# Performance work log

Hardware: AMD Instinct MI355X
Metric: run time of the kernel (lower is better)

Reference implementation:

```python
import jax, jax.numpy as jnp
import numpy as np

E = 1024  # embedding_dim
H = 64    # head_size

def setup_inputs() -> dict:
    key = jax.random.key(0)
    k1, k2, k3, k4 = jax.random.split(key, 4)
    x = jax.random.normal(k1, (4, 4096, E), dtype=jnp.float32)
    # nn.Linear(E, H, bias=False) weights have shape [H, E]; y = x @ W.T
    s = 1.0 / np.sqrt(E)
    Wq = jax.random.normal(k2, (H, E), dtype=jnp.float32) * s
    Wk = jax.random.normal(k3, (H, E), dtype=jnp.float32) * s
    Wv = jax.random.normal(k4, (H, E), dtype=jnp.float32) * s
    return {"x": x, "Wq": Wq, "Wk": Wk, "Wv": Wv}

def reference(x, Wq, Wk, Wv):
    B, T, E_ = x.shape
    q = jnp.einsum('bte,he->bth', x, Wq)
    k = jnp.einsum('bte,he->bth', x, Wk)
    v = jnp.einsum('bte,he->bth', x, Wv)
    # NOTE: original scales by sqrt(embedding_dim), not head_size
    scores = jnp.einsum('bqh,bkh->bqk', q, k) / jnp.sqrt(jnp.asarray(E_, x.dtype))
    causal = jnp.tril(jnp.ones((T, T), dtype=bool))
    scores = jnp.where(causal, scores, -jnp.inf)
    weights = jax.nn.softmax(scores, axis=-1)
    return jnp.einsum('bqk,bkh->bqh', weights, v)
```

## Files before the change

kernel.cpp:

```cpp
#include <hip/hip_runtime.h>
#include <stdint.h>

typedef __bf16 bf16x8 __attribute__((ext_vector_type(8)));
typedef float  f32x4  __attribute__((ext_vector_type(4)));

#define E_DIM 1024
#define H_DIM 64
#define T_SEQ 4096
#define B_BAT 4
#define M_TOT (B_BAT * T_SEQ)

__device__ __forceinline__ ushort f2bfu(float f) {
    return __builtin_bit_cast(ushort, (__bf16)f);
}
__device__ __forceinline__ uint32_t pk2(float lo, float hi) {
    return (uint32_t)f2bfu(lo) | ((uint32_t)f2bfu(hi) << 16);
}
__device__ __forceinline__ float ex2(float x) {
    return __builtin_amdgcn_exp2f(x);
}
__device__ __forceinline__ bf16x8 ldfrag(const ushort* p) {
    return __builtin_bit_cast(bf16x8, *(const uint4*)(p));
}
__device__ __forceinline__ void barrier_lgkm() {
    __builtin_amdgcn_s_waitcnt(0xC07F);
    __builtin_amdgcn_s_barrier();
}

__global__ __launch_bounds__(256) void wcvt(const float* __restrict__ Wq,
                                            const float* __restrict__ Wk,
                                            const float* __restrict__ Wv,
                                            ushort* __restrict__ Wfm) {
    int g = blockIdx.x * 256 + threadIdx.x;
    int n = g >> 7;
    int k8 = g & 127;
    const float* src = (n < 64) ? (Wq + (size_t)n * E_DIM)
                     : (n < 128) ? (Wk + (size_t)(n - 64) * E_DIM)
                     : (Wv + (size_t)(n - 128) * E_DIM);
    float sc = (n < 64) ? 0.045084220f : 1.0f;
    float4 a = *(const float4*)(src + k8 * 8);
    float4 b = *(const float4*)(src + k8 * 8 + 4);
    uint4 o;
    o.x = pk2(a.x * sc, a.y * sc); o.y = pk2(a.z * sc, a.w * sc);
    o.z = pk2(b.x * sc, b.y * sc); o.w = pk2(b.z * sc, b.w * sc);
    int s = k8 >> 3, kc = (k8 >> 2) & 1, qd = k8 & 3;
    int nt = n >> 4, lm = n & 15;
    int lane = qd * 16 + lm;
    *(uint4*)(Wfm + (((size_t)(s * 12 + nt) * 2 + kc) * 64 + lane) * 8) = o;
}

__global__ __launch_bounds__(256, 3) void qkv(const float* __restrict__ x,
                                              const ushort* __restrict__ Wfm,
                                              ushort* __restrict__ Qfm,
                                              ushort* __restrict__ Kfm,
                                              ushort* __restrict__ Vfm) {
    __shared__ union {
        ushort a[2][32 * 72];
        struct { ushort c[32 * 136]; ushort vt[64 * 40]; } epi;
    } sm;
    const int tid = threadIdx.x;
    const int w = tid >> 6, l = tid & 63;
    const int lm = l & 15, qd = l >> 4;
    const int m0 = blockIdx.x * 32;

    f32x4 acc[2][3];
#pragma unroll
    for (int r2 = 0; r2 < 2; ++r2)
#pragma unroll
        for (int t = 0; t < 3; ++t) acc[r2][t] = (f32x4){0.f, 0.f, 0.f, 0.f};

    const int srow = tid >> 3, kseg = tid & 7;
    const float* xsrc = x + (size_t)(m0 + srow) * E_DIM + kseg * 8;

    {
        float4 a0 = *(const float4*)xsrc;
        float4 a1 = *(const float4*)(xsrc + 4);
        uint4 u = {pk2(a0.x, a0.y), pk2(a0.z, a0.w), pk2(a1.x, a1.y), pk2(a1.z, a1.w)};
        *(uint4*)(&sm.a[0][srow * 72 + kseg * 8]) = u;
    }
    float4 xa0 = *(const float4*)(xsrc + 64);
    float4 xa1 = *(const float4*)(xsrc + 68);
    float4 xb0 = *(const float4*)(xsrc + 128);
    float4 xb1 = *(const float4*)(xsrc + 132);
    __syncthreads();

    for (int s = 0; s < 16; ++s) {
        const int cb = s & 1, nb = cb ^ 1;
        float4 xc0 = xa0, xc1 = xa1;
        if (s < 13) {
            xc0 = *(const float4*)(xsrc + (s + 3) * 64);
            xc1 = *(const float4*)(xsrc + (s + 3) * 64 + 4);
        }
        bf16x8 wf[3][2];
#pragma unroll
        for (int t = 0; t < 3; ++t)
#pragma unroll
            for (int kc = 0; kc < 2; ++kc)
                wf[t][kc] = ldfrag(Wfm + (((size_t)(s * 12 + w * 3 + t) * 2 + kc) * 64 + l) * 8);
        bf16x8 af[2][2];
#pragma unroll
        for (int r2 = 0; r2 < 2; ++r2)
#pragma unroll
            for (int kc = 0; kc < 2; ++kc)
                af[r2][kc] = ldfrag(&sm.a[cb][(r2 * 16 + lm) * 72 + kc * 32 + qd * 8]);
#pragma unroll
        for (int t = 0; t < 3; ++t)
#pragma unroll
            for (int kc = 0; kc < 2; ++kc)
#pragma unroll
                for (int r2 = 0; r2 < 2; ++r2)
                    acc[r2][t] = __builtin_amdgcn_mfma_f32_16x16x32_bf16(af[r2][kc], wf[t][kc], acc[r2][t], 0, 0, 0);
        if (s < 15) {
            uint4 u = {pk2(xa0.x, xa0.y), pk2(xa0.z, xa0.w), pk2(xa1.x, xa1.y), pk2(xa1.z, xa1.w)};
            *(uint4*)(&sm.a[nb][srow * 72 + kseg * 8]) = u;
        }
        xa0 = xb0; xa1 = xb1; xb0 = xc0; xb1 = xc1;
        if (s < 15) barrier_lgkm();
    }
    __syncthreads();

#pragma unroll
    for (int r2 = 0; r2 < 2; ++r2)
#pragma unroll
        for (int t = 0; t < 3; ++t) {
            int gc = w * 48 + t * 16 + lm;
            int m = r2 * 16 + qd * 4;
#pragma unroll
            for (int rr = 0; rr < 4; ++rr) {
                ushort v = f2bfu(acc[r2][t][rr]);
                if (gc < 128) sm.epi.c[(m + rr) * 136 + gc] = v;
                else          sm.epi.vt[(gc - 128) * 40 + (m + rr)] = v;
            }
        }
    __syncthreads();

    const int g16b = m0 >> 4;
    const int kt64 = m0 >> 6;
    const int tb   = (m0 >> 4) & 3;
    const int kcv  = (m0 >> 5) & 1;
#pragma unroll
    for (int ii = 0; ii < 3; ++ii) {
        int i = w + ii * 4;
        uint4 val;
        ushort* dst;
        if (i < 4) {
            int qt_l = i >> 1, kc = i & 1;
            val = *(const uint4*)(&sm.epi.c[(qt_l * 16 + lm) * 136 + kc * 32 + qd * 8]);
            dst = Qfm + (((size_t)(g16b + qt_l) * 2 + kc) * 64 + l) * 8;
        } else if (i < 8) {
            int j2 = i - 4, t_l = j2 >> 1, kc = j2 & 1;
            val = *(const uint4*)(&sm.epi.c[(t_l * 16 + lm) * 136 + 64 + kc * 32 + qd * 8]);
            dst = Kfm + (((size_t)((kt64 * 4 + tb + t_l) * 2 + kc)) * 64 + l) * 8;
        } else {
            int t = i - 8;
            val = *(const uint4*)(&sm.epi.vt[(t * 16 + lm) * 40 + qd * 8]);
            dst = Vfm + (((size_t)((kt64 * 4 + t) * 2 + kcv)) * 64 + l) * 8;
        }
        *(uint4*)dst = val;
    }
}

__global__ __launch_bounds__(256, 4) void flashc(const ushort* __restrict__ Qfm,
                                                 const ushort* __restrict__ Kfm,
                                                 const ushort* __restrict__ Vfm,
                                                 float* __restrict__ out) {
    __shared__ ushort plds[4][16 * 72];
    __shared__ float  ro[4][16][68];
    __shared__ float  rl[4][16];
    const int tid = threadIdx.x;
    const int wv = tid >> 6, l = tid & 63;
    const int lm = l & 15, qd = l >> 4;
    const int pr = blockIdx.x;
    const int bt = blockIdx.y;
    ushort* myp = plds[wv];

#pragma unroll 1
    for (int half = 0; half < 2; ++half) {
        const int j   = half ? (255 - pr) : pr;
        const int ktd = j >> 2;
        const int td  = j & 3;
        const int g16 = bt * 256 + j;

        bf16x8 qf0, qf1;
        {
            const ushort* qp = Qfm + ((size_t)g16 * 2) * 512 + l * 8;
            qf0 = ldfrag(qp);
            qf1 = ldfrag(qp + 512);
        }
        f32x4 o[4];
#pragma unroll
        for (int t = 0; t < 4; ++t) o[t] = (f32x4){0.f, 0.f, 0.f, 0.f};
        float lacc = 0.f;

#pragma unroll 1
        for (int kt = wv; kt <= ktd; kt += 4) {
            const ushort* kb = Kfm + ((size_t)(bt * 64 + kt) * 8) * 512;
            const ushort* vb = Vfm + ((size_t)(bt * 64 + kt) * 8) * 512;
            f32x4 sf[4];
#pragma unroll
            for (int t = 0; t < 4; ++t) sf[t] = (f32x4){0.f, 0.f, 0.f, 0.f};
#pragma unroll
            for (int t = 0; t < 4; ++t) {
                bf16x8 k0 = ldfrag(kb + (t * 2 + 0) * 512 + l * 8);
                bf16x8 k1 = ldfrag(kb + (t * 2 + 1) * 512 + l * 8);
                sf[t] = __builtin_amdgcn_mfma_f32_16x16x32_bf16(k0, qf0, sf[t], 0, 0, 0);
                sf[t] = __builtin_amdgcn_mfma_f32_16x16x32_bf16(k1, qf1, sf[t], 0, 0, 0);
            }
            uint4 vu[4][2];
#pragma unroll
            for (int t = 0; t < 4; ++t) {
                vu[t][0] = *(const uint4*)(vb + (t * 2 + 0) * 512 + l * 8);
                vu[t][1] = *(const uint4*)(vb + (t * 2 + 1) * 512 + l * 8);
            }
            ushort* wp = myp + lm * 72 + qd * 4;
            if (kt != ktd) {
#pragma unroll
                for (int t = 0; t < 4; ++t) {
                    float p0 = ex2(sf[t][0]), p1 = ex2(sf[t][1]);
                    float p2 = ex2(sf[t][2]), p3 = ex2(sf[t][3]);
                    lacc += (p0 + p1) + (p2 + p3);
                    *(uint2*)(wp + t * 16) = uint2{pk2(p0, p1), pk2(p2, p3)};
                }
            } else {
#pragma unroll
                for (int t = 0; t < 4; ++t) {
                    if (t < td) {
                        float p0 = ex2(sf[t][0]), p1 = ex2(sf[t][1]);
                        float p2 = ex2(sf[t][2]), p3 = ex2(sf[t][3]);
                        lacc += (p0 + p1) + (p2 + p3);
                        *(uint2*)(wp + t * 16) = uint2{pk2(p0, p1), pk2(p2, p3)};
                    } else if (t == td) {
                        float p[4];
#pragma unroll
                        for (int rr = 0; rr < 4; ++rr) {
                            float pe = ex2(sf[t][rr]);
                            if (qd * 4 + rr > lm) pe = 0.f;
                            lacc += pe;
                            p[rr] = pe;
                        }
                        *(uint2*)(wp + t * 16) = uint2{pk2(p[0], p[1]), pk2(p[2], p[3])};
                    } else {
                        *(uint2*)(wp + t * 16) = uint2{0u, 0u};
                    }
                }
            }
            __builtin_amdgcn_wave_barrier();
            __builtin_amdgcn_s_waitcnt(0xC07F);
            __builtin_amdgcn_wave_barrier();
            bf16x8 pf0 = ldfrag(myp + lm * 72 + qd * 8);
            bf16x8 pf1 = ldfrag(myp + lm * 72 + 32 + qd * 8);
#pragma unroll
            for (int t = 0; t < 4; ++t) {
                bf16x8 v0 = __builtin_bit_cast(bf16x8, vu[t][0]);
                bf16x8 v1 = __builtin_bit_cast(bf16x8, vu[t][1]);
                o[t] = __builtin_amdgcn_mfma_f32_16x16x32_bf16(pf0, v0, o[t], 0, 0, 0);
                o[t] = __builtin_amdgcn_mfma_f32_16x16x32_bf16(pf1, v1, o[t], 0, 0, 0);
            }
            __builtin_amdgcn_wave_barrier();
        }
        lacc += __shfl_xor(lacc, 16);
        lacc += __shfl_xor(lacc, 32);
        if (qd == 0) rl[wv][lm] = lacc;
#pragma unroll
        for (int t = 0; t < 4; ++t)
#pragma unroll
            for (int rr = 0; rr < 4; ++rr)
                ro[wv][qd * 4 + rr][t * 16 + lm] = o[t][rr];
        __syncthreads();
        {
            const int row = wv * 4 + qd;
            float ls = rl[0][row] + rl[1][row] + rl[2][row] + rl[3][row];
            float inv = 1.0f / ls;
            float4 s0 = *(const float4*)&ro[0][row][lm * 4];
            float4 s1 = *(const float4*)&ro[1][row][lm * 4];
            float4 s2 = *(const float4*)&ro[2][row][lm * 4];
            float4 s3 = *(const float4*)&ro[3][row][lm * 4];
            float4 ov;
            ov.x = (s0.x + s1.x + s2.x + s3.x) * inv;
            ov.y = (s0.y + s1.y + s2.y + s3.y) * inv;
            ov.z = (s0.z + s1.z + s2.z + s3.z) * inv;
            ov.w = (s0.w + s1.w + s2.w + s3.w) * inv;
            *(float4*)(out + ((size_t)bt * T_SEQ + j * 16 + row) * 64 + lm * 4) = ov;
        }
        __syncthreads();
    }
}

extern "C" void kernel_launch(void* const* d_in, const int* in_sizes, int n_in,
                              void* d_out, int out_size, void* d_ws, size_t ws_size,
                              hipStream_t stream) {
    const float* x  = (const float*)d_in[0];
    const float* Wq = (const float*)d_in[1];
    const float* Wk = (const float*)d_in[2];
    const float* Wv = (const float*)d_in[3];
    float* out = (float*)d_out;

    char* ws = (char*)d_ws;
    ushort* Wfm = (ushort*)(ws);
    ushort* Qfm = (ushort*)(ws + 393216);
    ushort* Kfm = (ushort*)(ws + 2490368);
    ushort* Vfm = (ushort*)(ws + 4587520);

    wcvt<<<96, 256, 0, stream>>>(Wq, Wk, Wv, Wfm);
    qkv<<<512, 256, 0, stream>>>(x, Wfm, Qfm, Kfm, Vfm);
    flashc<<<dim3(128, B_BAT), 256, 0, stream>>>(Qfm, Kfm, Vfm, out);
}
```

Measured before the change: 133.4 us.

## Fuse weight conversion, QKV projection and attention into one cooperative kernel

Merges the three kernels (weight convert, QKV projection, causal flash attention) into a single cooperative launch of 512 blocks, with grid-wide syncs between phases and a shared-memory union covering all three stages. The goal is to remove the launch gaps and inter-kernel tail idle between the stages. In exchange it adds two grid barriers, a larger union LDS footprint, and a launch bound of 2 blocks per CU. The attention phase is now tied to the same 512-block grid mapping (bid>>2, bid&3).

```diff
diff --git a/kernel.cpp b/kernel.cpp
--- a/kernel.cpp
+++ b/kernel.cpp
@@ -1,5 +1,8 @@
 #include <hip/hip_runtime.h>
+#include <hip/hip_cooperative_groups.h>
 #include <stdint.h>
+
+namespace cg = cooperative_groups;
 
 typedef __bf16 bf16x8 __attribute__((ext_vector_type(8)));
 typedef float  f32x4  __attribute__((ext_vector_type(4)));
@@ -27,262 +30,266 @@
     __builtin_amdgcn_s_barrier();
 }
 
-__global__ __launch_bounds__(256) void wcvt(const float* __restrict__ Wq,
-                                            const float* __restrict__ Wk,
-                                            const float* __restrict__ Wv,
-                                            ushort* __restrict__ Wfm) {
-    int g = blockIdx.x * 256 + threadIdx.x;
-    int n = g >> 7;
-    int k8 = g & 127;
-    const float* src = (n < 64) ? (Wq + (size_t)n * E_DIM)
-                     : (n < 128) ? (Wk + (size_t)(n - 64) * E_DIM)
-                     : (Wv + (size_t)(n - 128) * E_DIM);
-    float sc = (n < 64) ? 0.045084220f : 1.0f;
-    float4 a = *(const float4*)(src + k8 * 8);
-    float4 b = *(const float4*)(src + k8 * 8 + 4);
-    uint4 o;
-    o.x = pk2(a.x * sc, a.y * sc); o.y = pk2(a.z * sc, a.w * sc);
-    o.z = pk2(b.x * sc, b.y * sc); o.w = pk2(b.z * sc, b.w * sc);
-    int s = k8 >> 3, kc = (k8 >> 2) & 1, qd = k8 & 3;
-    int nt = n >> 4, lm = n & 15;
-    int lane = qd * 16 + lm;
-    *(uint4*)(Wfm + (((size_t)(s * 12 + nt) * 2 + kc) * 64 + lane) * 8) = o;
-}
-
-__global__ __launch_bounds__(256, 3) void qkv(const float* __restrict__ x,
-                                              const ushort* __restrict__ Wfm,
-                                              ushort* __restrict__ Qfm,
-                                              ushort* __restrict__ Kfm,
-                                              ushort* __restrict__ Vfm) {
+__global__ __launch_bounds__(256, 2) void fused_all(
+        const float* __restrict__ x,
+        const float* __restrict__ Wq, const float* __restrict__ Wk,
+        const float* __restrict__ Wv,
+        ushort* __restrict__ Wfm, ushort* __restrict__ Qfm,
+        ushort* __restrict__ Kfm, ushort* __restrict__ Vfm,
+        float* __restrict__ out) {
+    cg::grid_group grid = cg::this_grid();
     __shared__ union {
         ushort a[2][32 * 72];
         struct { ushort c[32 * 136]; ushort vt[64 * 40]; } epi;
+        struct { ushort plds[4][16 * 72];
+                 float  ro[4][16][68];
+                 float  rl[4][16]; } fl;
     } sm;
+
+    const int bid = blockIdx.x;
     const int tid = threadIdx.x;
     const int w = tid >> 6, l = tid & 63;
     const int lm = l & 15, qd = l >> 4;
-    const int m0 = blockIdx.x * 32;
-
-    f32x4 acc[2][3];
-#pragma unroll
-    for (int r2 = 0; r2 < 2; ++r2)
-#pragma unroll
-        for (int t = 0; t < 3; ++t) acc[r2][t] = (f32x4){0.f, 0.f, 0.f, 0.f};
-
-    const int srow = tid >> 3, kseg = tid & 7;
-    const float* xsrc = x + (size_t)(m0 + srow) * E_DIM + kseg * 8;
+
+    if (bid < 96) {
+        int g = bid * 256 + tid;
+        int n = g >> 7;
+        int k8 = g & 127;
+        const float* src = (n < 64) ? (Wq + (size_t)n * E_DIM)
+                         : (n < 128) ? (Wk + (size_t)(n - 64) * E_DIM)
+                         : (Wv + (size_t)(n - 128) * E_DIM);
+        float sc = (n < 64) ? 0.045084220f : 1.0f;
+        float4 a = *(const float4*)(src + k8 * 8);
+        float4 b = *(const float4*)(src + k8 * 8 + 4);
+        uint4 o;
+        o.x = pk2(a.x * sc, a.y * sc); o.y = pk2(a.z * sc, a.w * sc);
+        o.z = pk2(b.x * sc, b.y * sc); o.w = pk2(b.z * sc, b.w * sc);
+        int s = k8 >> 3, kc = (k8 >> 2) & 1, q4 = k8 & 3;
+        int nt = n >> 4, lmn = n & 15;
+        int lane = q4 * 16 + lmn;
+        *(uint4*)(Wfm + (((size_t)(s * 12 + nt) * 2 + kc) * 64 + lane) * 8) = o;
+    }
+    __threadfence();
+    grid.sync();
 
     {
-        float4 a0 = *(const float4*)xsrc;
-        float4 a1 = *(const float4*)(xsrc + 4);
-        uint4 u = {pk2(a0.x, a0.y), pk2(a0.z, a0.w), pk2(a1.x, a1.y), pk2(a1.z, a1.w)};
-        *(uint4*)(&sm.a[0][srow * 72 + kseg * 8]) = u;
+        const int m0 = bid * 32;
+
+        f32x4 acc[2][3];
+#pragma unroll
+        for (int r2 = 0; r2 < 2; ++r2)
+#pragma unroll
+            for (int t = 0; t < 3; ++t) acc[r2][t] = (f32x4){0.f, 0.f, 0.f, 0.f};
+
+        const int srow = tid >> 3, kseg = tid & 7;
+        const float* xsrc = x + (size_t)(m0 + srow) * E_DIM + kseg * 8;
+
+        {
+            float4 a0 = *(const float4*)xsrc;
+            float4 a1 = *(const float4*)(xsrc + 4);
+            uint4 u = {pk2(a0.x, a0.y), pk2(a0.z, a0.w), pk2(a1.x, a1.y), pk2(a1.z, a1.w)};
+            *(uint4*)(&sm.a[0][srow * 72 + kseg * 8]) = u;
+        }
+        float4 xa0 = *(const float4*)(xsrc + 64);
+        float4 xa1 = *(const float4*)(xsrc + 68);
+        float4 xb0 = *(const float4*)(xsrc + 128);
+        float4 xb1 = *(const float4*)(xsrc + 132);
+        __syncthreads();
+
+        for (int s = 0; s < 16; ++s) {
+            const int cb = s & 1, nb = cb ^ 1;
+            float4 xc0 = xa0, xc1 = xa1;
+            if (s < 13) {
+                xc0 = *(const float4*)(xsrc + (s + 3) * 64);
+                xc1 = *(const float4*)(xsrc + (s + 3) * 64 + 4);
+            }
+            bf16x8 wf[3][2];
+#pragma unroll
+            for (int t = 0; t < 3; ++t)
+#pragma unroll
+                for (int kc = 0; kc < 2; ++kc)
+                    wf[t][kc] = ldfrag(Wfm + (((size_t)(s * 12 + w * 3 + t) * 2 + kc) * 64 + l) * 8);
+            bf16x8 af[2][2];
+#pragma unroll
+            for (int r2 = 0; r2 < 2; ++r2)
+#pragma unroll
+                for (int kc = 0; kc < 2; ++kc)
+                    af[r2][kc] = ldfrag(&sm.a[cb][(r2 * 16 + lm) * 72 + kc * 32 + qd * 8]);
+#pragma unroll
+            for (int t = 0; t < 3; ++t)
+#pragma unroll
+                for (int kc = 0; kc < 2; ++kc)
+#pragma unroll
+                    for (int r2 = 0; r2 < 2; ++r2)
+                        acc[r2][t] = __builtin_amdgcn_mfma_f32_16x16x32_bf16(af[r2][kc], wf[t][kc], acc[r2][t], 0, 0, 0);
+            if (s < 15) {
+                uint4 u = {pk2(xa0.x, xa0.y), pk2(xa0.z, xa0.w), pk2(xa1.x, xa1.y), pk2(xa1.z, xa1.w)};
+                *(uint4*)(&sm.a[nb][srow * 72 + kseg * 8]) = u;
+            }
+            xa0 = xb0; xa1 = xb1; xb0 = xc0; xb1 = xc1;
+            if (s < 15) barrier_lgkm();
+        }
+        __syncthreads();
+
+#pragma unroll
+        for (int r2 = 0; r2 < 2; ++r2)
+#pragma unroll
+            for (int t = 0; t < 3; ++t) {
+                int gc = w * 48 + t * 16 + lm;
+                int m = r2 * 16 + qd * 4;
+#pragma unroll
+                for (int rr = 0; rr < 4; ++rr) {
+                    ushort v = f2bfu(acc[r2][t][rr]);
+                    if (gc < 128) sm.epi.c[(m + rr) * 136 + gc] = v;
+                    else          sm.epi.vt[(gc - 128) * 40 + (m + rr)] = v;
+                }
+            }
+        __syncthreads();
+
+        const int g16b = m0 >> 4;
+        const int kt64 = m0 >> 6;
+        const int tb   = (m0 >> 4) & 3;
+        const int kcv  = (m0 >> 5) & 1;
+#pragma unroll
+        for (int ii = 0; ii < 3; ++ii) {
+            int i = w + ii * 4;
+            uint4 val;
+            ushort* dst;
+            if (i < 4) {
+                int qt_l = i >> 1, kc = i & 1;
+                val = *(const uint4*)(&sm.epi.c[(qt_l * 16 + lm) * 136 + kc * 32 + qd * 8]);
+                dst = Qfm + (((size_t)(g16b + qt_l) * 2 + kc) * 64 + l) * 8;
+            } else if (i < 8) {
+                int j2 = i - 4, t_l = j2 >> 1, kc = j2 & 1;
+                val = *(const uint4*)(&sm.epi.c[(t_l * 16 + lm) * 136 + 64 + kc * 32 + qd * 8]);
+                dst = Kfm + (((size_t)((kt64 * 4 + tb + t_l) * 2 + kc)) * 64 + l) * 8;
+            } else {
+                int t = i - 8;
+                val = *(const uint4*)(&sm.epi.vt[(t * 16 + lm) * 40 + qd * 8]);
+                dst = Vfm + (((size_t)((kt64 * 4 + t) * 2 + kcv)) * 64 + l) * 8;
+            }
+            *(uint4*)dst = val;
+        }
     }
-    float4 xa0 = *(const float4*)(xsrc + 64);
-    float4 xa1 = *(const float4*)(xsrc + 68);
-    float4 xb0 = *(const float4*)(xsrc + 128);
-    float4 xb1 = *(const float4*)(xsrc + 132);
-    __syncthreads();
-
-    for (int s = 0; s < 16; ++s) {
-        const int cb = s & 1, nb = cb ^ 1;
-        float4 xc0 = xa0, xc1 = xa1;
-        if (s < 13) {
-            xc0 = *(const float4*)(xsrc + (s + 3) * 64);
-            xc1 = *(const float4*)(xsrc + (s + 3) * 64 + 4);
-        }
-        bf16x8 wf[3][2];
-#pragma unroll
-        for (int t = 0; t < 3; ++t)
-#pragma unroll
-            for (int kc = 0; kc < 2; ++kc)
-                wf[t][kc] = ldfrag(Wfm + (((size_t)(s * 12 + w * 3 + t) * 2 + kc) * 64 + l) * 8);
-        bf16x8 af[2][2];
-#pragma unroll
-        for (int r2 = 0; r2 < 2; ++r2)
-#pragma unroll
-            for (int kc = 0; kc < 2; ++kc)
-                af[r2][kc] = ldfrag(&sm.a[cb][(r2 * 16 + lm) * 72 + kc * 32 + qd * 8]);
-#pragma unroll
-        for (int t = 0; t < 3; ++t)
-#pragma unroll
-            for (int kc = 0; kc < 2; ++kc)
-#pragma unroll
-                for (int r2 = 0; r2 < 2; ++r2)
-                    acc[r2][t] = __builtin_amdgcn_mfma_f32_16x16x32_bf16(af[r2][kc], wf[t][kc], acc[r2][t], 0, 0, 0);
-        if (s < 15) {
-            uint4 u = {pk2(xa0.x, xa0.y), pk2(xa0.z, xa0.w), pk2(xa1.x, xa1.y), pk2(xa1.z, xa1.w)};
-            *(uint4*)(&sm.a[nb][srow * 72 + kseg * 8]) = u;
-        }
-        xa0 = xb0; xa1 = xb1; xb0 = xc0; xb1 = xc1;
-        if (s < 15) barrier_lgkm();
-    }
-    __syncthreads();
-
-#pragma unroll
-    for (int r2 = 0; r2 < 2; ++r2)
-#pragma unroll
-        for (int t = 0; t < 3; ++t) {
-            int gc = w * 48 + t * 16 + lm;
-            int m = r2 * 16 + qd * 4;
-#pragma unroll
-            for (int rr = 0; rr < 4; ++rr) {
-                ushort v = f2bfu(acc[r2][t][rr]);
-                if (gc < 128) sm.epi.c[(m + rr) * 136 + gc] = v;
-                else          sm.epi.vt[(gc - 128) * 40 + (m + rr)] = v;
-            }
-        }
-    __syncthreads();
-
-    const int g16b = m0 >> 4;
-    const int kt64 = m0 >> 6;
-    const int tb   = (m0 >> 4) & 3;
-    const int kcv  = (m0 >> 5) & 1;
-#pragma unroll
-    for (int ii = 0; ii < 3; ++ii) {
-        int i = w + ii * 4;
-        uint4 val;
-        ushort* dst;
-        if (i < 4) {
-            int qt_l = i >> 1, kc = i & 1;
-            val = *(const uint4*)(&sm.epi.c[(qt_l * 16 + lm) * 136 + kc * 32 + qd * 8]);
-            dst = Qfm + (((size_t)(g16b + qt_l) * 2 + kc) * 64 + l) * 8;
-        } else if (i < 8) {
-            int j2 = i - 4, t_l = j2 >> 1, kc = j2 & 1;
-            val = *(const uint4*)(&sm.epi.c[(t_l * 16 + lm) * 136 + 64 + kc * 32 + qd * 8]);
-            dst = Kfm + (((size_t)((kt64 * 4 + tb + t_l) * 2 + kc)) * 64 + l) * 8;
-        } else {
-            int t = i - 8;
-            val = *(const uint4*)(&sm.epi.vt[(t * 16 + lm) * 40 + qd * 8]);
-            dst = Vfm + (((size_t)((kt64 * 4 + t) * 2 + kcv)) * 64 + l) * 8;
-        }
-        *(uint4*)dst = val;
-    }
-}
-
-__global__ __launch_bounds__(256, 4) void flashc(const ushort* __restrict__ Qfm,
-                                                 const ushort* __restrict__ Kfm,
-                                                 const ushort* __restrict__ Vfm,
-                                                 float* __restrict__ out) {
-    __shared__ ushort plds[4][16 * 72];
-    __shared__ float  ro[4][16][68];
-    __shared__ float  rl[4][16];
-    const int tid = threadIdx.x;
-    const int wv = tid >> 6, l = tid & 63;
-    const int lm = l & 15, qd = l >> 4;
-    const int pr = blockIdx.x;
-    const int bt = blockIdx.y;
-    ushort* myp = plds[wv];
+    __threadfence();
+    grid.sync();
+
+    {
+        const int pr = bid >> 2;
+        const int bt = bid & 3;
+        const int wv = w;
+        ushort* myp = sm.fl.plds[wv];
 
 #pragma unroll 1
-    for (int half = 0; half < 2; ++half) {
-        const int j   = half ? (255 - pr) : pr;
-        const int ktd = j >> 2;
-        const int td  = j & 3;
-        const int g16 = bt * 256 + j;
-
-        bf16x8 qf0, qf1;
-        {
-            const ushort* qp = Qfm + ((size_t)g16 * 2) * 512 + l * 8;
-            qf0 = ldfrag(qp);
-            qf1 = ldfrag(qp + 512);
-        }
-        f32x4 o[4];
-#pragma unroll
-        for (int t = 0; t < 4; ++t) o[t] = (f32x4){0.f, 0.f, 0.f, 0.f};
-        float lacc = 0.f;
+        for (int half = 0; half < 2; ++half) {
+            const int j   = half ? (255 - pr) : pr;
+            const int ktd = j >> 2;
+            const int td  = j & 3;
+            const int g16 = bt * 256 + j;
+
+            bf16x8 qf0, qf1;
+            {
+                const ushort* qp = Qfm + ((size_t)g16 * 2) * 512 + l * 8;
+                qf0 = ldfrag(qp);
+                qf1 = ldfrag(qp + 512);
+            }
+            f32x4 o[4];
+#pragma unroll
+            for (int t = 0; t < 4; ++t) o[t] = (f32x4){0.f, 0.f, 0.f, 0.f};
+            float lacc = 0.f;
 
 #pragma unroll 1
-        for (int kt = wv; kt <= ktd; kt += 4) {
-            const ushort* kb = Kfm + ((size_t)(bt * 64 + kt) * 8) * 512;
-            const ushort* vb = Vfm + ((size_t)(bt * 64 + kt) * 8) * 512;
-            f32x4 sf[4];
-#pragma unroll
-            for (int t = 0; t < 4; ++t) sf[t] = (f32x4){0.f, 0.f, 0.f, 0.f};
-#pragma unroll
-            for (int t = 0; t < 4; ++t) {
-                bf16x8 k0 = ldfrag(kb + (t * 2 + 0) * 512 + l * 8);
-                bf16x8 k1 = ldfrag(kb + (t * 2 + 1) * 512 + l * 8);
-                sf[t] = __builtin_amdgcn_mfma_f32_16x16x32_bf16(k0, qf0, sf[t], 0, 0, 0);
-                sf[t] = __builtin_amdgcn_mfma_f32_16x16x32_bf16(k1, qf1, sf[t], 0, 0, 0);
-            }
-            uint4 vu[4][2];
-#pragma unroll
-            for (int t = 0; t < 4; ++t) {
-                vu[t][0] = *(const uint4*)(vb + (t * 2 + 0) * 512 + l * 8);
-                vu[t][1] = *(const uint4*)(vb + (t * 2 + 1) * 512 + l * 8);
-            }
-            ushort* wp = myp + lm * 72 + qd * 4;
-            if (kt != ktd) {
+            for (int kt = wv; kt <= ktd; kt += 4) {
+                const ushort* kb = Kfm + ((size_t)(bt * 64 + kt) * 8) * 512;
+                const ushort* vb = Vfm + ((size_t)(bt * 64 + kt) * 8) * 512;
+                f32x4 sf[4];
+#pragma unroll
+                for (int t = 0; t < 4; ++t) sf[t] = (f32x4){0.f, 0.f, 0.f, 0.f};
 #pragma unroll
                 for (int t = 0; t < 4; ++t) {
-                    float p0 = ex2(sf[t][0]), p1 = ex2(sf[t][1]);
-                    float p2 = ex2(sf[t][2]), p3 = ex2(sf[t][3]);
-                    lacc += (p0 + p1) + (p2 + p3);
-                    *(uint2*)(wp + t * 16) = uint2{pk2(p0, p1), pk2(p2, p3)};
-                }
-            } else {
+                    bf16x8 k0 = ldfrag(kb + (t * 2 + 0) * 512 + l * 8);
+                    bf16x8 k1 = ldfrag(kb + (t * 2 + 1) * 512 + l * 8);
+                    sf[t] = __builtin_amdgcn_mfma_f32_16x16x32_bf16(k0, qf0, sf[t], 0, 0, 0);
+                    sf[t] = __builtin_amdgcn_mfma_f32_16x16x32_bf16(k1, qf1, sf[t], 0, 0, 0);
+                }
+                uint4 vu[4][2];
 #pragma unroll
                 for (int t = 0; t < 4; ++t) {
-                    if (t < td) {
+                    vu[t][0] = *(const uint4*)(vb + (t * 2 + 0) * 512 + l * 8);
+                    vu[t][1] = *(const uint4*)(vb + (t * 2 + 1) * 512 + l * 8);
+                }
+                ushort* wp = myp + lm * 72 + qd * 4;
+                if (kt != ktd) {
+#pragma unroll
+                    for (int t = 0; t < 4; ++t) {
                         float p0 = ex2(sf[t][0]), p1 = ex2(sf[t][1]);
                         float p2 = ex2(sf[t][2]), p3 = ex2(sf[t][3]);
                         lacc += (p0 + p1) + (p2 + p3);
                         *(uint2*)(wp + t * 16) = uint2{pk2(p0, p1), pk2(p2, p3)};
-                    } else if (t == td) {
-                        float p[4];
-#pragma unroll
-                        for (int rr = 0; rr < 4; ++rr) {
-                            float pe = ex2(sf[t][rr]);
-                            if (qd * 4 + rr > lm) pe = 0.f;
-                            lacc += pe;
-                            p[rr] = pe;
+                    }
+                } else {
+#pragma unroll
+                    for (int t = 0; t < 4; ++t) {
+                        if (t < td) {
+                            float p0 = ex2(sf[t][0]), p1 = ex2(sf[t][1]);
+                            float p2 = ex2(sf[t][2]), p3 = ex2(sf[t][3]);
+                            lacc += (p0 + p1) + (p2 + p3);
+                            *(uint2*)(wp + t * 16) = uint2{pk2(p0, p1), pk2(p2, p3)};
+                        } else if (t == td) {
+                            float p[4];
+#pragma unroll
+                            for (int rr = 0; rr < 4; ++rr) {
+                                float pe = ex2(sf[t][rr]);
+                                if (qd * 4 + rr > lm) pe = 0.f;
+                                lacc += pe;
+                                p[rr] = pe;
+                            }
+                            *(uint2*)(wp + t * 16) = uint2{pk2(p[0], p[1]), pk2(p[2], p[3])};
+                        } else {
+                            *(uint2*)(wp + t * 16) = uint2{0u, 0u};
                         }
-                        *(uint2*)(wp + t * 16) = uint2{pk2(p[0], p[1]), pk2(p[2], p[3])};
-                    } else {
-                        *(uint2*)(wp + t * 16) = uint2{0u, 0u};
                     }
                 }
-            }
-            __builtin_amdgcn_wave_barrier();
-            __builtin_amdgcn_s_waitcnt(0xC07F);
-            __builtin_amdgcn_wave_barrier();
-            bf16x8 pf0 = ldfrag(myp + lm * 72 + qd * 8);
-            bf16x8 pf1 = ldfrag(myp + lm * 72 + 32 + qd * 8);
-#pragma unroll
-            for (int t = 0; t < 4; ++t) {
-                bf16x8 v0 = __builtin_bit_cast(bf16x8, vu[t][0]);
-                bf16x8 v1 = __builtin_bit_cast(bf16x8, vu[t][1]);
-                o[t] = __builtin_amdgcn_mfma_f32_16x16x32_bf16(pf0, v0, o[t], 0, 0, 0);
-                o[t] = __builtin_amdgcn_mfma_f32_16x16x32_bf16(pf1, v1, o[t], 0, 0, 0);
-            }
-            __builtin_amdgcn_wave_barrier();
+                __builtin_amdgcn_wave_barrier();
+                __builtin_amdgcn_s_waitcnt(0xC07F);
+                __builtin_amdgcn_wave_barrier();
+                bf16x8 pf0 = ldfrag(myp + lm * 72 + qd * 8);
+                bf16x8 pf1 = ldfrag(myp + lm * 72 + 32 + qd * 8);
+#pragma unroll
+                for (int t = 0; t < 4; ++t) {
+                    bf16x8 v0 = __builtin_bit_cast(bf16x8, vu[t][0]);
+                    bf16x8 v1 = __builtin_bit_cast(bf16x8, vu[t][1]);
+                    o[t] = __builtin_amdgcn_mfma_f32_16x16x32_bf16(pf0, v0, o[t], 0, 0, 0);
+                    o[t] = __builtin_amdgcn_mfma_f32_16x16x32_bf16(pf1, v1, o[t], 0, 0, 0);
+                }
+                __builtin_amdgcn_wave_barrier();
+            }
+            lacc += __shfl_xor(lacc, 16);
+            lacc += __shfl_xor(lacc, 32);
+            if (qd == 0) sm.fl.rl[wv][lm] = lacc;
+#pragma unroll
+            for (int t = 0; t < 4; ++t)
+#pragma unroll
+                for (int rr = 0; rr < 4; ++rr)
+                    sm.fl.ro[wv][qd * 4 + rr][t * 16 + lm] = o[t][rr];
+            __syncthreads();
+            {
+                const int row = wv * 4 + qd;
+                float ls = sm.fl.rl[0][row] + sm.fl.rl[1][row] + sm.fl.rl[2][row] + sm.fl.rl[3][row];
+                float inv = 1.0f / ls;
+                float4 s0 = *(const float4*)&sm.fl.ro[0][row][lm * 4];
+                float4 s1 = *(const float4*)&sm.fl.ro[1][row][lm * 4];
+                float4 s2 = *(const float4*)&sm.fl.ro[2][row][lm * 4];
+                float4 s3 = *(const float4*)&sm.fl.ro[3][row][lm * 4];
+                float4 ov;
+                ov.x = (s0.x + s1.x + s2.x + s3.x) * inv;
+                ov.y = (s0.y + s1.y + s2.y + s3.y) * inv;
+                ov.z = (s0.z + s1.z + s2.z + s3.z) * inv;
+                ov.w = (s0.w + s1.w + s2.w + s3.w) * inv;
+                *(float4*)(out + ((size_t)bt * T_SEQ + j * 16 + row) * 64 + lm * 4) = ov;
+            }
+            __syncthreads();
         }
-        lacc += __shfl_xor(lacc, 16);
-        lacc += __shfl_xor(lacc, 32);
-        if (qd == 0) rl[wv][lm] = lacc;
-#pragma unroll
-        for (int t = 0; t < 4; ++t)
-#pragma unroll
-            for (int rr = 0; rr < 4; ++rr)
-                ro[wv][qd * 4 + rr][t * 16 + lm] = o[t][rr];
-        __syncthreads();
-        {
-            const int row = wv * 4 + qd;
-            float ls = rl[0][row] + rl[1][row] + rl[2][row] + rl[3][row];
-            float inv = 1.0f / ls;
-            float4 s0 = *(const float4*)&ro[0][row][lm * 4];
-            float4 s1 = *(const float4*)&ro[1][row][lm * 4];
-            float4 s2 = *(const float4*)&ro[2][row][lm * 4];
-            float4 s3 = *(const float4*)&ro[3][row][lm * 4];
-            float4 ov;
-            ov.x = (s0.x + s1.x + s2.x + s3.x) * inv;
-            ov.y = (s0.y + s1.y + s2.y + s3.y) * inv;
-            ov.z = (s0.z + s1.z + s2.z + s3.z) * inv;
-            ov.w = (s0.w + s1.w + s2.w + s3.w) * inv;
-            *(float4*)(out + ((size_t)bt * T_SEQ + j * 16 + row) * 64 + lm * 4) = ov;
-        }
-        __syncthreads();
     }
 }
 
@@ -301,7 +308,9 @@
     ushort* Kfm = (ushort*)(ws + 2490368);
     ushort* Vfm = (ushort*)(ws + 4587520);
 
-    wcvt<<<96, 256, 0, stream>>>(Wq, Wk, Wv, Wfm);
-    qkv<<<512, 256, 0, stream>>>(x, Wfm, Qfm, Kfm, Vfm);
-    flashc<<<dim3(128, B_BAT), 256, 0, stream>>>(Qfm, Kfm, Vfm, out);
-}
+    void* args[] = { (void*)&x, (void*)&Wq, (void*)&Wk, (void*)&Wv,
+                     (void*)&Wfm, (void*)&Qfm, (void*)&Kfm, (void*)&Vfm,
+                     (void*)&out };
+    hipLaunchCooperativeKernel((const void*)fused_all, dim3(512), dim3(256),
+                               args, 0, stream);
+}
```

Measured after the change: 363.8 us. 173% more time.

## Process both paired query tiles together to share K/V loads

Applied to the files above, without the earlier changes.

The flash kernel now handles the two query tiles of a block (pr and 255-pr) at the same time instead of one after the other. Each K and V tile is loaded once and used for both query tiles over the shared prefix, which roughly halves global K/V traffic for that range. The cost is more registers (two sets of accumulators and Q fragments), so launch bounds drop from 4 to 2 blocks per CU. The P buffer is doubled and shares a union with the reduction buffers.

```diff
diff --git a/kernel.cpp b/kernel.cpp
--- a/kernel.cpp
+++ b/kernel.cpp
@@ -160,129 +160,186 @@
     }
 }
 
-__global__ __launch_bounds__(256, 4) void flashc(const ushort* __restrict__ Qfm,
+__global__ __launch_bounds__(256, 2) void flashm(const ushort* __restrict__ Qfm,
                                                  const ushort* __restrict__ Kfm,
                                                  const ushort* __restrict__ Vfm,
                                                  float* __restrict__ out) {
-    __shared__ ushort plds[4][16 * 72];
-    __shared__ float  ro[4][16][68];
-    __shared__ float  rl[4][16];
+    __shared__ union {
+        ushort plds[4][2][16 * 72];
+        struct { float ro[4][16][68]; float rl[4][16]; } red;
+    } sm;
     const int tid = threadIdx.x;
     const int wv = tid >> 6, l = tid & 63;
     const int lm = l & 15, qd = l >> 4;
     const int pr = blockIdx.x;
     const int bt = blockIdx.y;
-    ushort* myp = plds[wv];
-
+    const int jA = pr, jB = 255 - pr;
+    const int ktdA = jA >> 2, tdA = jA & 3;
+    const int ktdB = jB >> 2, tdB = jB & 3;
+    ushort* mypA = sm.plds[wv][0];
+    ushort* mypB = sm.plds[wv][1];
+
+    bf16x8 qA0, qA1, qB0, qB1;
+    {
+        const ushort* qp = Qfm + ((size_t)(bt * 256 + jA) * 2) * 512 + l * 8;
+        qA0 = ldfrag(qp); qA1 = ldfrag(qp + 512);
+        const ushort* qq = Qfm + ((size_t)(bt * 256 + jB) * 2) * 512 + l * 8;
+        qB0 = ldfrag(qq); qB1 = ldfrag(qq + 512);
+    }
+    f32x4 oA[4], oB[4];
+#pragma unroll
+    for (int t = 0; t < 4; ++t) {
+        oA[t] = (f32x4){0.f, 0.f, 0.f, 0.f};
+        oB[t] = (f32x4){0.f, 0.f, 0.f, 0.f};
+    }
+    float laccA = 0.f, laccB = 0.f;
+
+    auto emitP = [&](const f32x4* sf, ushort* wp, bool diag, int td, float& lacc) {
+#pragma unroll
+        for (int t = 0; t < 4; ++t) {
+            if (!diag || t < td) {
+                float p0 = ex2(sf[t][0]), p1 = ex2(sf[t][1]);
+                float p2 = ex2(sf[t][2]), p3 = ex2(sf[t][3]);
+                lacc += (p0 + p1) + (p2 + p3);
+                *(uint2*)(wp + t * 16) = uint2{pk2(p0, p1), pk2(p2, p3)};
+            } else if (t == td) {
+                float p[4];
+#pragma unroll
+                for (int rr = 0; rr < 4; ++rr) {
+                    float pe = ex2(sf[t][rr]);
+                    if (qd * 4 + rr > lm) pe = 0.f;
+                    lacc += pe;
+                    p[rr] = pe;
+                }
+                *(uint2*)(wp + t * 16) = uint2{pk2(p[0], p[1]), pk2(p[2], p[3])};
+            } else {
+                *(uint2*)(wp + t * 16) = uint2{0u, 0u};
+            }
+        }
+    };
+    auto pv = [&](const ushort* myp, const uint4 (&vu)[4][2], f32x4* o) {
+        bf16x8 p0 = ldfrag(myp + lm * 72 + qd * 8);
+        bf16x8 p1 = ldfrag(myp + lm * 72 + 32 + qd * 8);
+#pragma unroll
+        for (int t = 0; t < 4; ++t) {
+            bf16x8 v0 = __builtin_bit_cast(bf16x8, vu[t][0]);
+            bf16x8 v1 = __builtin_bit_cast(bf16x8, vu[t][1]);
+            o[t] = __builtin_amdgcn_mfma_f32_16x16x32_bf16(p0, v0, o[t], 0, 0, 0);
+            o[t] = __builtin_amdgcn_mfma_f32_16x16x32_bf16(p1, v1, o[t], 0, 0, 0);
+        }
+    };
+
+    int kt = wv;
 #pragma unroll 1
-    for (int half = 0; half < 2; ++half) {
-        const int j   = half ? (255 - pr) : pr;
-        const int ktd = j >> 2;
-        const int td  = j & 3;
-        const int g16 = bt * 256 + j;
-
-        bf16x8 qf0, qf1;
-        {
-            const ushort* qp = Qfm + ((size_t)g16 * 2) * 512 + l * 8;
-            qf0 = ldfrag(qp);
-            qf1 = ldfrag(qp + 512);
-        }
-        f32x4 o[4];
-#pragma unroll
-        for (int t = 0; t < 4; ++t) o[t] = (f32x4){0.f, 0.f, 0.f, 0.f};
-        float lacc = 0.f;
-
+    for (; kt <= ktdA; kt += 4) {
+        const ushort* kb = Kfm + ((size_t)(bt * 64 + kt) * 8) * 512;
+        const ushort* vb = Vfm + ((size_t)(bt * 64 + kt) * 8) * 512;
+        f32x4 sfA[4], sfB[4];
+#pragma unroll
+        for (int t = 0; t < 4; ++t) {
+            sfA[t] = (f32x4){0.f, 0.f, 0.f, 0.f};
+            sfB[t] = (f32x4){0.f, 0.f, 0.f, 0.f};
+        }
+#pragma unroll
+        for (int t = 0; t < 4; ++t) {
+            bf16x8 k0 = ldfrag(kb + (t * 2 + 0) * 512 + l * 8);
+            bf16x8 k1 = ldfrag(kb + (t * 2 + 1) * 512 + l * 8);
+            sfB[t] = __builtin_amdgcn_mfma_f32_16x16x32_bf16(k0, qB0, sfB[t], 0, 0, 0);
+            sfB[t] = __builtin_amdgcn_mfma_f32_16x16x32_bf16(k1, qB1, sfB[t], 0, 0, 0);
+            sfA[t] = __builtin_amdgcn_mfma_f32_16x16x32_bf16(k0, qA0, sfA[t], 0, 0, 0);
+            sfA[t] = __builtin_amdgcn_mfma_f32_16x16x32_bf16(k1, qA1, sfA[t], 0, 0, 0);
+        }
+        uint4 vu[4][2];
+#pragma unroll
+        for (int t = 0; t < 4; ++t) {
+            vu[t][0] = *(const uint4*)(vb + (t * 2 + 0) * 512 + l * 8);
+            vu[t][1] = *(const uint4*)(vb + (t * 2 + 1) * 512 + l * 8);
+        }
+        emitP(sfB, mypB + lm * 72 + qd * 4, false, tdB, laccB);
+        emitP(sfA, mypA + lm * 72 + qd * 4, kt == ktdA, tdA, laccA);
+        __builtin_amdgcn_wave_barrier();
+        __builtin_amdgcn_s_waitcnt(0xC07F);
+        __builtin_amdgcn_wave_barrier();
+        pv(mypB, vu, oB);
+        pv(mypA, vu, oA);
+        __builtin_amdgcn_wave_barrier();
+    }
 #pragma unroll 1
-        for (int kt = wv; kt <= ktd; kt += 4) {
-            const ushort* kb = Kfm + ((size_t)(bt * 64 + kt) * 8) * 512;
-            const ushort* vb = Vfm + ((size_t)(bt * 64 + kt) * 8) * 512;
-            f32x4 sf[4];
-#pragma unroll
-            for (int t = 0; t < 4; ++t) sf[t] = (f32x4){0.f, 0.f, 0.f, 0.f};
-#pragma unroll
-            for (int t = 0; t < 4; ++t) {
-                bf16x8 k0 = ldfrag(kb + (t * 2 + 0) * 512 + l * 8);
-                bf16x8 k1 = ldfrag(kb + (t * 2 + 1) * 512 + l * 8);
-                sf[t] = __builtin_amdgcn_mfma_f32_16x16x32_bf16(k0, qf0, sf[t], 0, 0, 0);
-                sf[t] = __builtin_amdgcn_mfma_f32_16x16x32_bf16(k1, qf1, sf[t], 0, 0, 0);
-            }
-            uint4 vu[4][2];
-#pragma unroll
-            for (int t = 0; t < 4; ++t) {
-                vu[t][0] = *(const uint4*)(vb + (t * 2 + 0) * 512 + l * 8);
-                vu[t][1] = *(const uint4*)(vb + (t * 2 + 1) * 512 + l * 8);
-            }
-            ushort* wp = myp + lm * 72 + qd * 4;
-            if (kt != ktd) {
-#pragma unroll
-                for (int t = 0; t < 4; ++t) {
-                    float p0 = ex2(sf[t][0]), p1 = ex2(sf[t][1]);
-                    float p2 = ex2(sf[t][2]), p3 = ex2(sf[t][3]);
-                    lacc += (p0 + p1) + (p2 + p3);
-                    *(uint2*)(wp + t * 16) = uint2{pk2(p0, p1), pk2(p2, p3)};
-                }
-            } else {
-#pragma unroll
-                for (int t = 0; t < 4; ++t) {
-                    if (t < td) {
-                        float p0 = ex2(sf[t][0]), p1 = ex2(sf[t][1]);
-                        float p2 = ex2(sf[t][2]), p3 = ex2(sf[t][3]);
-                        lacc += (p0 + p1) + (p2 + p3);
-                        *(uint2*)(wp + t * 16) = uint2{pk2(p0, p1), pk2(p2, p3)};
-                    } else if (t == td) {
-                        float p[4];
-#pragma unroll
-                        for (int rr = 0; rr < 4; ++rr) {
-                            float pe = ex2(sf[t][rr]);
-                            if (qd * 4 + rr > lm) pe = 0.f;
-                            lacc += pe;
-                            p[rr] = pe;
-                        }
-                        *(uint2*)(wp + t * 16) = uint2{pk2(p[0], p[1]), pk2(p[2], p[3])};
-                    } else {
-                        *(uint2*)(wp + t * 16) = uint2{0u, 0u};
-                    }
-                }
-            }
-            __builtin_amdgcn_wave_barrier();
-            __builtin_amdgcn_s_waitcnt(0xC07F);
-            __builtin_amdgcn_wave_barrier();
-            bf16x8 pf0 = ldfrag(myp + lm * 72 + qd * 8);
-            bf16x8 pf1 = ldfrag(myp + lm * 72 + 32 + qd * 8);
-#pragma unroll
-            for (int t = 0; t < 4; ++t) {
-                bf16x8 v0 = __builtin_bit_cast(bf16x8, vu[t][0]);
-                bf16x8 v1 = __builtin_bit_cast(bf16x8, vu[t][1]);
-                o[t] = __builtin_amdgcn_mfma_f32_16x16x32_bf16(pf0, v0, o[t], 0, 0, 0);
-                o[t] = __builtin_amdgcn_mfma_f32_16x16x32_bf16(pf1, v1, o[t], 0, 0, 0);
-            }
-            __builtin_amdgcn_wave_barrier();
-        }
-        lacc += __shfl_xor(lacc, 16);
-        lacc += __shfl_xor(lacc, 32);
-        if (qd == 0) rl[wv][lm] = lacc;
-#pragma unroll
-        for (int t = 0; t < 4; ++t)
-#pragma unroll
-            for (int rr = 0; rr < 4; ++rr)
-                ro[wv][qd * 4 + rr][t * 16 + lm] = o[t][rr];
-        __syncthreads();
-        {
-            const int row = wv * 4 + qd;
-            float ls = rl[0][row] + rl[1][row] + rl[2][row] + rl[3][row];
-            float inv = 1.0f / ls;
-            float4 s0 = *(const float4*)&ro[0][row][lm * 4];
-            float4 s1 = *(const float4*)&ro[1][row][lm * 4];
-            float4 s2 = *(const float4*)&ro[2][row][lm * 4];
-            float4 s3 = *(const float4*)&ro[3][row][lm * 4];
-            float4 ov;
-            ov.x = (s0.x + s1.x + s2.x + s3.x) * inv;
-            ov.y = (s0.y + s1.y + s2.y + s3.y) * inv;
-            ov.z = (s0.z + s1.z + s2.z + s3.z) * inv;
-            ov.w = (s0.w + s1.w + s2.w + s3.w) * inv;
-            *(float4*)(out + ((size_t)bt * T_SEQ + j * 16 + row) * 64 + lm * 4) = ov;
-        }
-        __syncthreads();
+    for (; kt <= ktdB; kt += 4) {
+        const ushort* kb = Kfm + ((size_t)(bt * 64 + kt) * 8) * 512;
+        const ushort* vb = Vfm + ((size_t)(bt * 64 + kt) * 8) * 512;
+        f32x4 sfB[4];
+#pragma unroll
+        for (int t = 0; t < 4; ++t) sfB[t] = (f32x4){0.f, 0.f, 0.f, 0.f};
+#pragma unroll
+        for (int t = 0; t < 4; ++t) {
+            bf16x8 k0 = ldfrag(kb + (t * 2 + 0) * 512 + l * 8);
+            bf16x8 k1 = ldfrag(kb + (t * 2 + 1) * 512 + l * 8);
+            sfB[t] = __builtin_amdgcn_mfma_f32_16x16x32_bf16(k0, qB0, sfB[t], 0, 0, 0);
+            sfB[t] = __builtin_amdgcn_mfma_f32_16x16x32_bf16(k1, qB1, sfB[t], 0, 0, 0);
+        }
+        uint4 vu[4][2];
+#pragma unroll
+        for (int t = 0; t < 4; ++t) {
+            vu[t][0] = *(const uint4*)(vb + (t * 2 + 0) * 512 + l * 8);
+            vu[t][1] = *(const uint4*)(vb + (t * 2 + 1) * 512 + l * 8);
+        }
+        emitP(sfB, mypB + lm * 72 + qd * 4, kt == ktdB, tdB, laccB);
+        __builtin_amdgcn_wave_barrier();
+        __builtin_amdgcn_s_waitcnt(0xC07F);
+        __builtin_amdgcn_wave_barrier();
+        pv(mypB, vu, oB);
+        __builtin_amdgcn_wave_barrier();
+    }
+
+    laccA += __shfl_xor(laccA, 16); laccA += __shfl_xor(laccA, 32);
+    laccB += __shfl_xor(laccB, 16); laccB += __shfl_xor(laccB, 32);
+
+    __syncthreads();
+    if (qd == 0) sm.red.rl[wv][lm] = laccA;
+#pragma unroll
+    for (int t = 0; t < 4; ++t)
+#pragma unroll
+        for (int rr = 0; rr < 4; ++rr)
+            sm.red.ro[wv][qd * 4 + rr][t * 16 + lm] = oA[t][rr];
+    __syncthreads();
+    {
+        const int row = wv * 4 + qd;
+        float ls = sm.red.rl[0][row] + sm.red.rl[1][row] + sm.red.rl[2][row] + sm.red.rl[3][row];
+        float inv = 1.0f / ls;
+        float4 s0 = *(const float4*)&sm.red.ro[0][row][lm * 4];
+        float4 s1 = *(const float4*)&sm.red.ro[1][row][lm * 4];
+        float4 s2 = *(const float4*)&sm.red.ro[2][row][lm * 4];
+        float4 s3 = *(const float4*)&sm.red.ro[3][row][lm * 4];
+        float4 ov;
+        ov.x = (s0.x + s1.x + s2.x + s3.x) * inv;
+        ov.y = (s0.y + s1.y + s2.y + s3.y) * inv;
+        ov.z = (s0.z + s1.z + s2.z + s3.z) * inv;
+        ov.w = (s0.w + s1.w + s2.w + s3.w) * inv;
+        *(float4*)(out + ((size_t)bt * T_SEQ + jA * 16 + row) * 64 + lm * 4) = ov;
+    }
+    __syncthreads();
+    if (qd == 0) sm.red.rl[wv][lm] = laccB;
+#pragma unroll
+    for (int t = 0; t < 4; ++t)
+#pragma unroll
+        for (int rr = 0; rr < 4; ++rr)
+            sm.red.ro[wv][qd * 4 + rr][t * 16 + lm] = oB[t][rr];
+    __syncthreads();
+    {
+        const int row = wv * 4 + qd;
+        float ls = sm.red.rl[0][row] + sm.red.rl[1][row] + sm.red.rl[2][row] + sm.red.rl[3][row];
+        float inv = 1.0f / ls;
+        float4 s0 = *(const float4*)&sm.red.ro[0][row][lm * 4];
+        float4 s1 = *(const float4*)&sm.red.ro[1][row][lm * 4];
+        float4 s2 = *(const float4*)&sm.red.ro[2][row][lm * 4];
+        float4 s3 = *(const float4*)&sm.red.ro[3][row][lm * 4];
+        float4 ov;
+        ov.x = (s0.x + s1.x + s2.x + s3.x) * inv;
+        ov.y = (s0.y + s1.y + s2.y + s3.y) * inv;
+        ov.z = (s0.z + s1.z + s2.z + s3.z) * inv;
+        ov.w = (s0.w + s1.w + s2.w + s3.w) * inv;
+        *(float4*)(out + ((size_t)bt * T_SEQ + jB * 16 + row) * 64 + lm * 4) = ov;
     }
 }
 
@@ -303,5 +360,5 @@
 
     wcvt<<<96, 256, 0, stream>>>(Wq, Wk, Wv, Wfm);
     qkv<<<512, 256, 0, stream>>>(x, Wfm, Qfm, Kfm, Vfm);
-    flashc<<<dim3(128, B_BAT), 256, 0, stream>>>(Qfm, Kfm, Vfm, out);
-}
+    flashm<<<dim3(128, B_BAT), 256, 0, stream>>>(Qfm, Kfm, Vfm, out);
+}
```

New measurement: 132.8 us. No clear change (-0.4%).
